# Performance work log

Measured on AMD Instinct MI355X. Metric: run time of the kernel, lower is better.

## Reference

```python
import math
import jax, jax.numpy as jnp
import numpy as np

B, L, C, H = 4, 2048, 1024, 16
D = C // H


def setup_inputs() -> dict:
    key = jax.random.key(0)
    k1, k2, k3 = jax.random.split(key, 3)
    x = jax.random.normal(k1, (B, L, C), dtype=jnp.float32)
    Wqkv = jax.random.normal(k2, (C, 3 * C), dtype=jnp.float32) * (1.0 / math.sqrt(C))
    bqkv = jax.random.normal(k3, (3 * C,), dtype=jnp.float32) * 0.02
    return {"x": x, "Wqkv": Wqkv, "bqkv": bqkv}


def reference(x, Wqkv, bqkv):
    b, l, c = x.shape
    h, d = H, c // H
    qkv = x @ Wqkv + bqkv                      # [B, L, 3C]
    q, k, v = jnp.split(qkv, 3, axis=-1)
    # [B, L, C] -> [B, H, L, D]
    q = q.reshape(b, l, h, d).transpose(0, 2, 1, 3)
    k = k.reshape(b, l, h, d).transpose(0, 2, 1, 3)
    v = v.reshape(b, l, h, d).transpose(0, 2, 1, 3)
    scale = 1.0 / math.sqrt(d)
    scores = jnp.einsum('bhld,bhmd->bhlm', q, k) * scale  # [B, H, L, L]
    causal = jnp.tril(jnp.ones((l, l), dtype=bool))       # [L, L]
    scores = jnp.where(causal[None, None, :, :], scores, -jnp.inf)
    attn = jax.nn.softmax(scores, axis=-1)
    y = jnp.einsum('bhlm,bhmd->bhld', attn, v)            # [B, H, L, D]
    y = y.transpose(0, 2, 1, 3).reshape(b, l, c)          # [B, L, C]
    return y
```

## Files before the change

### kernel.cpp

```cpp
#include <hip/hip_runtime.h>

#define L_SEQ 2048
#define CDIM  1024
#define NH    16
#define HD    64
#define NBH   64
#define KDIM  1024

typedef __attribute__((ext_vector_type(4))) float f32x4;
typedef __attribute__((ext_vector_type(8))) short s16x8;
typedef __attribute__((ext_vector_type(4))) short s16x4;

__device__ inline short f2bf(float f) {
  union { float f; unsigned u; } v; v.f = f;
  unsigned r = v.u + 0x7fffu + ((v.u >> 16) & 1u);
  return (short)(r >> 16);
}

__device__ inline f32x4 mfma16(s16x8 a, s16x8 b, f32x4 c) {
  return __builtin_amdgcn_mfma_f32_16x16x32_bf16(a, b, c, 0, 0, 0);
}

__device__ inline unsigned cvt_pk_bf16(float lo, float hi) {
  unsigned r;
  asm("v_cvt_pk_bf16_f32 %0, %1, %2" : "=v"(r) : "v"(lo), "v"(hi));
  return r;
}

__device__ inline void gload_lds16(const short* g, short* l) {
  __builtin_amdgcn_global_load_lds(
      (const __attribute__((address_space(1))) unsigned*)g,
      (__attribute__((address_space(3))) unsigned*)l, 16, 0, 0);
}

__global__ __launch_bounds__(256) void convert_f32_bf16(const float* __restrict__ in,
                                                        short* __restrict__ out) {
  int i = (blockIdx.x * 256 + threadIdx.x) * 4;
  typedef __attribute__((ext_vector_type(4))) float fv4;
  fv4 v = *(const fv4*)(in + i);
  s16x4 o;
  o[0] = f2bf(v[0]); o[1] = f2bf(v[1]); o[2] = f2bf(v[2]); o[3] = f2bf(v[3]);
  *(s16x4*)(out + i) = o;
}

__global__ __launch_bounds__(256) void transpose_w(const float* __restrict__ W,
                                                   short* __restrict__ Wt) {
  __shared__ float tile[64][65];
  int n0 = blockIdx.x * 64, k0 = blockIdx.y * 64;
  int tc = threadIdx.x & 63, tr = threadIdx.x >> 6;
#pragma unroll
  for (int i = 0; i < 16; ++i) {
    int r = i * 4 + tr;
    tile[r][tc] = W[(size_t)(k0 + r) * 3072 + n0 + tc];
  }
  __syncthreads();
#pragma unroll
  for (int i = 0; i < 16; ++i) {
    int r = i * 4 + tr;
    Wt[(size_t)(n0 + r) * 1024 + k0 + tc] = f2bf(tile[tc][r]);
  }
}

__global__ __launch_bounds__(256) void transpose_v(const short* __restrict__ V,
                                                   short* __restrict__ Vt) {
  __shared__ short tile[64][72];
  int bh = blockIdx.y, l0 = blockIdx.x * 64;
  const short* Vb = V + (size_t)bh * L_SEQ * HD;
  short* Vtb = Vt + (size_t)bh * HD * L_SEQ;
  int tc = threadIdx.x & 63, tr = threadIdx.x >> 6;
#pragma unroll
  for (int i = 0; i < 16; ++i) {
    int r = i * 4 + tr;
    tile[r][tc] = Vb[(size_t)(l0 + r) * HD + tc];
  }
  __syncthreads();
#pragma unroll
  for (int i = 0; i < 16; ++i) {
    int r = i * 4 + tr;
    Vtb[(size_t)r * L_SEQ + l0 + tc] = tile[tc][r];
  }
}

__global__ __launch_bounds__(256) void qkv_gemm(const short* __restrict__ A,
                                                const short* __restrict__ Bt,
                                                const float* __restrict__ bias,
                                                short* __restrict__ Qo,
                                                short* __restrict__ Ko,
                                                short* __restrict__ Vo) {
  __shared__ __align__(16) short As[128 * 64];
  __shared__ __align__(16) short Bs[128 * 64];
  const int t = threadIdx.x;
  const int lane = t & 63, wid = t >> 6;
  const int wm = wid >> 1, wn = wid & 1;
  const int lrow = lane & 15, lg = lane >> 4;
  const int tm = blockIdx.x * 128, tn = blockIdx.y * 128;

  const int srow = lane >> 3;
  const int schunk = (lane & 7) ^ srow;
  const int sw = lrow & 7;

  f32x4 acc[4][4];
#pragma unroll
  for (int i = 0; i < 4; ++i)
#pragma unroll
    for (int j = 0; j < 4; ++j) { acc[i][j][0]=0.f; acc[i][j][1]=0.f; acc[i][j][2]=0.f; acc[i][j][3]=0.f; }

  for (int kt = 0; kt < KDIM; kt += 64) {
    __syncthreads();
#pragma unroll
    for (int ii = 0; ii < 4; ++ii) {
      int row0 = wid * 32 + ii * 8;
      int rowg = row0 + srow;
      gload_lds16(A  + (size_t)(tm + rowg) * KDIM + kt + schunk * 8, &As[row0 * 64]);
      gload_lds16(Bt + (size_t)(tn + rowg) * KDIM + kt + schunk * 8, &Bs[row0 * 64]);
    }
    asm volatile("s_waitcnt vmcnt(0)" ::: "memory");
    __syncthreads();

    s16x8 af[4][2], bf[4][2];
#pragma unroll
    for (int i = 0; i < 4; ++i) {
      int row = wm * 64 + i * 16 + lrow;
      af[i][0] = *(const s16x8*)(As + row * 64 + ((lg)     ^ sw) * 8);
      af[i][1] = *(const s16x8*)(As + row * 64 + ((4 + lg) ^ sw) * 8);
    }
#pragma unroll
    for (int j = 0; j < 4; ++j) {
      int row = wn * 64 + j * 16 + lrow;
      bf[j][0] = *(const s16x8*)(Bs + row * 64 + ((lg)     ^ sw) * 8);
      bf[j][1] = *(const s16x8*)(Bs + row * 64 + ((4 + lg) ^ sw) * 8);
    }
#pragma unroll
    for (int i = 0; i < 4; ++i)
#pragma unroll
      for (int j = 0; j < 4; ++j) {
        acc[i][j] = mfma16(af[i][0], bf[j][0], acc[i][j]);
        acc[i][j] = mfma16(af[i][1], bf[j][1], acc[i][j]);
      }
  }

  const float QS = 0.125f * 1.4426950408889634f;
#pragma unroll
  for (int i = 0; i < 4; ++i)
#pragma unroll
    for (int j = 0; j < 4; ++j) {
      int n = tn + wn * 64 + j * 16 + lrow;
      float bv = bias[n];
      int s = n >> 10, rem = n & 1023;
      int h = rem >> 6, d = rem & 63;
#pragma unroll
      for (int r = 0; r < 4; ++r) {
        int m = tm + wm * 64 + i * 16 + lg * 4 + r;
        int b = m >> 11, l = m & 2047;
        float v = acc[i][j][r] + bv;
        size_t idx = ((size_t)(b * NH + h) * L_SEQ + l) * HD + d;
        if (s == 0)      Qo[idx] = f2bf(v * QS);
        else if (s == 1) Ko[idx] = f2bf(v);
        else             Vo[idx] = f2bf(v);
      }
    }
}

__global__ __launch_bounds__(256) void attn(const short* __restrict__ Q,
                                            const short* __restrict__ K,
                                            const short* __restrict__ Vt,
                                            float* __restrict__ out) {
  const int t = threadIdx.x, lane = t & 63, wid = t >> 6;
  const int lrow = lane & 15, lg = lane >> 4;
  const int bh = blockIdx.y;
  const size_t bhoff = (size_t)bh * L_SEQ * HD;
  const short* Qb = Q + bhoff;
  const short* Kb = K + bhoff;
  const short* Vb = Vt + (size_t)bh * HD * L_SEQ;
  const int b = bh >> 4, h = bh & 15;
  const int src0 = lrow + ((lane & 16) << 1);
  const int src1 = src0 + 16;
  const bool hi_nf = (lg & 2) != 0;

#pragma unroll
  for (int tt = 0; tt < 2; ++tt) {
    const int qt = tt ? (31 - (int)blockIdx.x) : (int)blockIdx.x;
    const int q0 = qt * 64 + wid * 16;
    const int qi = q0 + lrow;

    s16x8 qf0 = *(const s16x8*)(Qb + (size_t)qi * HD + lg * 8);
    s16x8 qf1 = *(const s16x8*)(Qb + (size_t)qi * HD + 32 + lg * 8);

    f32x4 o[4];
#pragma unroll
    for (int dt = 0; dt < 4; ++dt) { o[dt][0]=0.f; o[dt][1]=0.f; o[dt][2]=0.f; o[dt][3]=0.f; }
    float mr = -1e30f, lr = 0.f;

    const int kvend = q0 + 16;
    for (int kv0 = 0; kv0 < kvend; kv0 += 64) {
      s16x8 vf[2][4];
#pragma unroll
      for (int ks = 0; ks < 2; ++ks)
#pragma unroll
        for (int dt = 0; dt < 4; ++dt)
          vf[ks][dt] = *(const s16x8*)(Vb + (size_t)(dt * 16 + lrow) * L_SEQ + kv0 + ks * 32 + lg * 8);

      f32x4 s[4];
#pragma unroll
      for (int nf = 0; nf < 4; ++nf) {
        f32x4 sv; sv[0]=0.f; sv[1]=0.f; sv[2]=0.f; sv[3]=0.f;
        const short* Krow = Kb + (size_t)(kv0 + nf * 16 + lrow) * HD;
        sv = mfma16(*(const s16x8*)(Krow + lg * 8), qf0, sv);
        sv = mfma16(*(const s16x8*)(Krow + 32 + lg * 8), qf1, sv);
        s[nf] = sv;
      }
      if (kv0 + 63 > q0) {
#pragma unroll
        for (int nf = 0; nf < 4; ++nf)
#pragma unroll
          for (int r = 0; r < 4; ++r)
            if (kv0 + nf * 16 + lg * 4 + r > qi) s[nf][r] = -INFINITY;
      }
      float mt = s[0][0];
#pragma unroll
      for (int nf = 0; nf < 4; ++nf)
#pragma unroll
        for (int r = 0; r < 4; ++r) mt = fmaxf(mt, s[nf][r]);
      mt = fmaxf(mt, __shfl_xor(mt, 16));
      mt = fmaxf(mt, __shfl_xor(mt, 32));
      float mn = fmaxf(mr, mt);
      float fr = exp2f(mr - mn);
      mr = mn;
      float ps = 0.f;
#pragma unroll
      for (int nf = 0; nf < 4; ++nf)
#pragma unroll
        for (int r = 0; r < 4; ++r) {
          float p = exp2f(s[nf][r] - mn);
          s[nf][r] = p; ps += p;
        }
      ps += __shfl_xor(ps, 16);
      ps += __shfl_xor(ps, 32);
      lr = lr * fr + ps;
#pragma unroll
      for (int dt = 0; dt < 4; ++dt) o[dt] *= fr;

      unsigned w0[4], w1[4];
#pragma unroll
      for (int nf = 0; nf < 4; ++nf) {
        w0[nf] = cvt_pk_bf16(s[nf][0], s[nf][1]);
        w1[nf] = cvt_pk_bf16(s[nf][2], s[nf][3]);
      }

#pragma unroll
      for (int ks = 0; ks < 2; ++ks) {
        int a0 = __shfl((int)w0[2 * ks],     src0);
        int a1 = __shfl((int)w0[2 * ks + 1], src0);
        int b0 = __shfl((int)w1[2 * ks],     src0);
        int b1 = __shfl((int)w1[2 * ks + 1], src0);
        int c0 = __shfl((int)w0[2 * ks],     src1);
        int c1 = __shfl((int)w0[2 * ks + 1], src1);
        int d0 = __shfl((int)w1[2 * ks],     src1);
        int d1 = __shfl((int)w1[2 * ks + 1], src1);
        union { int i[4]; s16x8 v; } pu;
        pu.i[0] = hi_nf ? a1 : a0;
        pu.i[1] = hi_nf ? b1 : b0;
        pu.i[2] = hi_nf ? c1 : c0;
        pu.i[3] = hi_nf ? d1 : d0;
#pragma unroll
        for (int dt = 0; dt < 4; ++dt)
          o[dt] = mfma16(vf[ks][dt], pu.v, o[dt]);
      }
    }

    const float inv = 1.0f / lr;
    const size_t obase = (size_t)(b * L_SEQ + qi) * CDIM + h * HD + lg * 4;
#pragma unroll
    for (int dt = 0; dt < 4; ++dt) {
      f32x4 ov = o[dt] * inv;
      *(f32x4*)(out + obase + dt * 16) = ov;
    }
  }
}

extern "C" void kernel_launch(void* const* d_in, const int* in_sizes, int n_in,
                              void* d_out, int out_size, void* d_ws, size_t ws_size,
                              hipStream_t stream) {
  const float* x    = (const float*)d_in[0];
  const float* W    = (const float*)d_in[1];
  const float* bqkv = (const float*)d_in[2];
  float* out = (float*)d_out;
  char* ws = (char*)d_ws;

  const size_t SZ_XB  = (size_t)8192 * 1024 * 2;
  const size_t SZ_WT  = (size_t)3072 * 1024 * 2;
  const size_t SZ_HEAD = (size_t)NBH * L_SEQ * HD * 2;

  short* xb  = (short*)ws;
  short* wtb = (short*)(ws + SZ_XB);
  short* Qo  = (short*)(ws + SZ_XB + SZ_WT);
  short* Ko  = (short*)(ws + SZ_XB + SZ_WT + SZ_HEAD);
  short* Vo  = (short*)(ws + SZ_XB + SZ_WT + 2 * SZ_HEAD);
  short* Vtb = (short*)ws;

  convert_f32_bf16<<<8192, 256, 0, stream>>>(x, xb);
  transpose_w<<<dim3(48, 16), 256, 0, stream>>>(W, wtb);
  qkv_gemm<<<dim3(64, 24), 256, 0, stream>>>(xb, wtb, bqkv, Qo, Ko, Vo);
  transpose_v<<<dim3(32, 64), 256, 0, stream>>>(Vo, Vtb);
  attn<<<dim3(16, 64), 256, 0, stream>>>(Qo, Ko, Vtb, out);
}
```

Before: 400.0 us.

## Fuse V transpose into QKV GEMM epilogue and remap attention blocks per XCD

Removes the separate V transpose kernel by having the QKV GEMM epilogue write V directly in [bh, d, l] layout. The attention launch becomes a 1D grid whose block index is decoded so that all blocks of the same heads land on the same XCD, which should improve L2 reuse of K and V. The transposed V stores in the epilogue are strided by the sequence length and may coalesce poorly.

Measured after the change: 404.1 us. No clear change (+1.0%).

```diff
diff --git a/kernel.cpp b/kernel.cpp
--- a/kernel.cpp
+++ b/kernel.cpp
@@ -61,32 +61,12 @@
   }
 }
 
-__global__ __launch_bounds__(256) void transpose_v(const short* __restrict__ V,
-                                                   short* __restrict__ Vt) {
-  __shared__ short tile[64][72];
-  int bh = blockIdx.y, l0 = blockIdx.x * 64;
-  const short* Vb = V + (size_t)bh * L_SEQ * HD;
-  short* Vtb = Vt + (size_t)bh * HD * L_SEQ;
-  int tc = threadIdx.x & 63, tr = threadIdx.x >> 6;
-#pragma unroll
-  for (int i = 0; i < 16; ++i) {
-    int r = i * 4 + tr;
-    tile[r][tc] = Vb[(size_t)(l0 + r) * HD + tc];
-  }
-  __syncthreads();
-#pragma unroll
-  for (int i = 0; i < 16; ++i) {
-    int r = i * 4 + tr;
-    Vtb[(size_t)r * L_SEQ + l0 + tc] = tile[tc][r];
-  }
-}
-
 __global__ __launch_bounds__(256) void qkv_gemm(const short* __restrict__ A,
                                                 const short* __restrict__ Bt,
                                                 const float* __restrict__ bias,
                                                 short* __restrict__ Qo,
                                                 short* __restrict__ Ko,
-                                                short* __restrict__ Vo) {
+                                                short* __restrict__ Vt) {
   __shared__ __align__(16) short As[128 * 64];
   __shared__ __align__(16) short Bs[128 * 64];
   const int t = threadIdx.x;
@@ -153,10 +133,13 @@
         int m = tm + wm * 64 + i * 16 + lg * 4 + r;
         int b = m >> 11, l = m & 2047;
         float v = acc[i][j][r] + bv;
-        size_t idx = ((size_t)(b * NH + h) * L_SEQ + l) * HD + d;
-        if (s == 0)      Qo[idx] = f2bf(v * QS);
-        else if (s == 1) Ko[idx] = f2bf(v);
-        else             Vo[idx] = f2bf(v);
+        if (s == 0) {
+          Qo[((size_t)(b * NH + h) * L_SEQ + l) * HD + d] = f2bf(v * QS);
+        } else if (s == 1) {
+          Ko[((size_t)(b * NH + h) * L_SEQ + l) * HD + d] = f2bf(v);
+        } else {
+          Vt[((size_t)(b * NH + h) * HD + d) * L_SEQ + l] = f2bf(v);
+        }
       }
     }
 }
@@ -167,7 +150,10 @@
                                             float* __restrict__ out) {
   const int t = threadIdx.x, lane = t & 63, wid = t >> 6;
   const int lrow = lane & 15, lg = lane >> 4;
-  const int bh = blockIdx.y;
+  const int n = blockIdx.x;
+  const int xcd = n & 7, slot = n >> 3;
+  const int bh = xcd * 8 + (slot >> 4);
+  const int qp = slot & 15;
   const size_t bhoff = (size_t)bh * L_SEQ * HD;
   const short* Qb = Q + bhoff;
   const short* Kb = K + bhoff;
@@ -179,7 +165,7 @@
 
 #pragma unroll
   for (int tt = 0; tt < 2; ++tt) {
-    const int qt = tt ? (31 - (int)blockIdx.x) : (int)blockIdx.x;
+    const int qt = tt ? (31 - qp) : qp;
     const int q0 = qt * 64 + wid * 16;
     const int qi = q0 + lrow;
 
@@ -295,12 +281,10 @@
   short* wtb = (short*)(ws + SZ_XB);
   short* Qo  = (short*)(ws + SZ_XB + SZ_WT);
   short* Ko  = (short*)(ws + SZ_XB + SZ_WT + SZ_HEAD);
-  short* Vo  = (short*)(ws + SZ_XB + SZ_WT + 2 * SZ_HEAD);
-  short* Vtb = (short*)ws;
+  short* Vtb = (short*)(ws + SZ_XB + SZ_WT + 2 * SZ_HEAD);
 
   convert_f32_bf16<<<8192, 256, 0, stream>>>(x, xb);
   transpose_w<<<dim3(48, 16), 256, 0, stream>>>(W, wtb);
-  qkv_gemm<<<dim3(64, 24), 256, 0, stream>>>(xb, wtb, bqkv, Qo, Ko, Vo);
-  transpose_v<<<dim3(32, 64), 256, 0, stream>>>(Vo, Vtb);
-  attn<<<dim3(16, 64), 256, 0, stream>>>(Qo, Ko, Vtb, out);
-}
+  qkv_gemm<<<dim3(64, 24), 256, 0, stream>>>(xb, wtb, bqkv, Qo, Ko, Vtb);
+  attn<<<1024, 256, 0, stream>>>(Qo, Ko, Vtb, out);
+}
```
